# Optimization experiments

Hardware: AMD Instinct MI355X
Metric: run time of the kernel (lower is better)

## Reference

```python
import jax, jax.numpy as jnp
import numpy as np

N_NODES = 50000
N_EDGES = 1600000
D = 128
L = 4
N_GRAPHS = 512


def setup_inputs() -> dict:
    key = jax.random.key(0)
    ks = jax.random.split(key, 8)
    x = jax.random.normal(ks[0], (N_NODES, D), dtype=jnp.float32)
    edge_index = jax.random.randint(ks[1], (2, N_EDGES), 0, N_NODES, dtype=jnp.int64)
    batch = jnp.sort(jax.random.randint(ks[2], (N_NODES,), 0, N_GRAPHS, dtype=jnp.int64))
    # MLP params per GIN layer: Linear(D->D), ReLU, Linear(D->D). Stacked over L layers.
    s = 1.0 / np.sqrt(D)
    Ws1 = jax.random.uniform(ks[3], (L, D, D), jnp.float32, -s, s)
    bs1 = jax.random.uniform(ks[4], (L, D), jnp.float32, -s, s)
    Ws2 = jax.random.uniform(ks[5], (L, D, D), jnp.float32, -s, s)
    bs2 = jax.random.uniform(ks[6], (L, D), jnp.float32, -s, s)
    return {"x": x, "edge_index": edge_index, "batch": batch,
            "Ws1": Ws1, "bs1": bs1, "Ws2": Ws2, "bs2": bs2}


def reference(x, edge_index, batch, Ws1, bs1, Ws2, bs2):
    src, dst = edge_index[0], edge_index[1]
    for l in range(L):
        # GINConv (eps=0): h = MLP(x + sum_{j in N(i)} x_j)
        agg = jax.ops.segment_sum(x[src], dst, num_segments=N_NODES)  # [N, D]
        h = x + agg
        h = jax.nn.relu(h @ Ws1[l] + bs1[l])
        x = h @ Ws2[l] + bs2[l]
    # global_add_pool: segment-sum node features by graph id
    return jax.ops.segment_sum(x, batch, num_segments=N_GRAPHS)  # [G, D]
```

## Files before the change

kernel.cpp:

```cpp
#include <hip/hip_runtime.h>

#define NN 50000
#define NE 1600000
#define DD 128
#define NL 4
#define NG 512
#define BSH 7
#define BMSK 127
#define NBUK 391
#define NBLK 196
#define EPB 8192
#define HN (NBUK * NBLK)
#define HT 150
#define EPT 20
#define CVT_N (NN * DD / 4)
#define PREP_N (NL * DD * DD)

typedef __attribute__((ext_vector_type(8))) short short8;
typedef __attribute__((ext_vector_type(4))) float floatx4;

__device__ __forceinline__ unsigned short f2bf(float f) {
    unsigned int u = __float_as_uint(f);
    u += 0x7fffu + ((u >> 16) & 1u);
    return (unsigned short)(u >> 16);
}
__device__ __forceinline__ float bf2f(unsigned short u) {
    return __uint_as_float(((unsigned int)u) << 16);
}

__global__ __launch_bounds__(512) void prelude_kernel(
    const float* __restrict__ x0, const float* __restrict__ Ws1,
    const float* __restrict__ Ws2, const int* __restrict__ dst,
    unsigned short* __restrict__ xbf, unsigned short* __restrict__ W1T,
    unsigned short* __restrict__ W2T, int* __restrict__ hist) {
    __shared__ int h[NBUK];
    int tid = threadIdx.x, bid = blockIdx.x;
    int gid = bid * 512 + tid;
    for (int idx = gid; idx < CVT_N; idx += NBLK * 512) {
        float4 f = ((const float4*)x0)[idx];
        ushort4 o;
        o.x = f2bf(f.x); o.y = f2bf(f.y); o.z = f2bf(f.z); o.w = f2bf(f.w);
        ((ushort4*)xbf)[idx] = o;
    }
    for (int idx = gid; idx < PREP_N; idx += NBLK * 512) {
        int l = idx >> 14, rem = idx & 16383;
        int k = rem >> 7, n = rem & 127;
        int o = (l << 14) + (n << 7) + k;
        W1T[o] = f2bf(Ws1[idx]);
        W2T[o] = f2bf(Ws2[idx]);
    }
    for (int i = tid; i < NBUK; i += 512) h[i] = 0;
    __syncthreads();
    {
        int base = bid * EPB;
        int end = base + EPB; if (end > NE) end = NE;
        for (int e = base + tid; e < end; e += 512) atomicAdd(&h[dst[e] >> BSH], 1);
    }
    __syncthreads();
    for (int i = tid; i < NBUK; i += 512) hist[i * NBLK + bid] = h[i];
}

__global__ __launch_bounds__(512) void scan_lb_kernel(const int* __restrict__ in,
                                                      int* __restrict__ out,
                                                      unsigned int* __restrict__ tstat,
                                                      int n) {
    __shared__ int s[512];
    int b = blockIdx.x, tid = threadIdx.x;
    int i = b * 512 + tid;
    int v = (i < n) ? in[i] : 0;
    s[tid] = v;
    __syncthreads();
    for (int off = 1; off < 512; off <<= 1) {
        int u = (tid >= off) ? s[tid - off] : 0;
        __syncthreads();
        s[tid] += u;
        __syncthreads();
    }
    int incl = s[tid];
    int agg = s[511];
    if (tid == 0)
        __hip_atomic_store(&tstat[b], 0x80000000u | (unsigned int)agg,
                           __ATOMIC_RELAXED, __HIP_MEMORY_SCOPE_AGENT);
    unsigned int got = 0;
    if (tid < b) {
        unsigned int x = __hip_atomic_load(&tstat[tid], __ATOMIC_RELAXED,
                                           __HIP_MEMORY_SCOPE_AGENT);
        while (!(x & 0x80000000u)) {
            __builtin_amdgcn_s_sleep(1);
            x = __hip_atomic_load(&tstat[tid], __ATOMIC_RELAXED,
                                  __HIP_MEMORY_SCOPE_AGENT);
        }
        got = x & 0x7FFFFFFFu;
    }
    __syncthreads();
    s[tid] = (int)got;
    __syncthreads();
    for (int off = 256; off > 0; off >>= 1) {
        if (tid < off) s[tid] += s[tid + off];
        __syncthreads();
    }
    int carry = s[0];
    if (i < n) out[i] = carry + incl - v;
}

__global__ __launch_bounds__(512) void bscatter_kernel(const int* __restrict__ src,
                                                       const int* __restrict__ dst,
                                                       const int* __restrict__ bkoff,
                                                       int* __restrict__ ebuf) {
    __shared__ int h[NBUK];
    int tid = threadIdx.x;
    for (int i = tid; i < NBUK; i += 512) h[i] = 0;
    __syncthreads();
    int base = blockIdx.x * EPB;
#pragma unroll
    for (int it = 0; it < EPB / 512; it++) {
        int e = base + it * 512 + tid;
        if (e < NE) {
            int d = dst[e];
            int bu = d >> BSH;
            int p = atomicAdd(&h[bu], 1);
            ebuf[bkoff[bu * NBLK + blockIdx.x] + p] = (src[e] << BSH) | (d & BMSK);
        }
    }
}

__global__ __launch_bounds__(256) void bucket_csr_kernel(const int* __restrict__ ebuf,
                                                         const int* __restrict__ bkoff,
                                                         int* __restrict__ rowptr,
                                                         int* __restrict__ rowend,
                                                         int* __restrict__ col) {
    __shared__ int cnt[128], exc[128], ebase[128];
    int b = blockIdx.x, tid = threadIdx.x;
    int segstart = bkoff[b * NBLK];
    int segend = (b < NBUK - 1) ? bkoff[(b + 1) * NBLK] : NE;
    if (tid < 128) cnt[tid] = 0;
    __syncthreads();
    int evr[EPT];
    int rnk[EPT];
#pragma unroll
    for (int j = 0; j < EPT; j++) {
        int i = segstart + tid + j * 256;
        if (i < segend) {
            int ev = ebuf[i];
            evr[j] = ev;
            rnk[j] = atomicAdd(&cnt[ev & BMSK], 1);
        } else {
            evr[j] = -1;
        }
    }
    __syncthreads();
    int v = (tid < 128) ? cnt[tid] : 0;
    if (tid < 128) exc[tid] = v;
    __syncthreads();
    for (int off = 1; off < 128; off <<= 1) {
        int u = (tid < 128 && tid >= off) ? exc[tid - off] : 0;
        __syncthreads();
        if (tid < 128) exc[tid] += u;
        __syncthreads();
    }
    if (tid < 128) {
        int excl = exc[tid] - v;
        ebase[tid] = segstart + excl;
        int node = (b << BSH) + tid;
        if (node < NN) {
            rowptr[node] = segstart + excl;
            rowend[node] = segstart + excl + v;
        }
    }
    __syncthreads();
#pragma unroll
    for (int j = 0; j < EPT; j++) {
        if (evr[j] >= 0) {
            int low = evr[j] & BMSK;
            col[ebase[low] + rnk[j]] = ((unsigned)evr[j]) >> BSH;
        }
    }
}

__global__ __launch_bounds__(256) void agg_kernel(const unsigned short* __restrict__ xbf,
                                                  const int* __restrict__ rowptr,
                                                  const int* __restrict__ rowend,
                                                  const int* __restrict__ col,
                                                  unsigned short* __restrict__ hpre) {
    int g = threadIdx.x >> 4;
    int lane = threadIdx.x & 15;
    int node = blockIdx.x * 16 + g;
    const uint4* base = (const uint4*)xbf;
    float a[8];
    {
        uint4 v = base[node * 16 + lane];
        a[0] = __uint_as_float(v.x << 16); a[1] = __uint_as_float(v.x & 0xFFFF0000u);
        a[2] = __uint_as_float(v.y << 16); a[3] = __uint_as_float(v.y & 0xFFFF0000u);
        a[4] = __uint_as_float(v.z << 16); a[5] = __uint_as_float(v.z & 0xFFFF0000u);
        a[6] = __uint_as_float(v.w << 16); a[7] = __uint_as_float(v.w & 0xFFFF0000u);
    }
    int s = rowptr[node], e = rowend[node];
    int i = s;
    for (; i + 8 <= e; i += 8) {
        uint4 v0 = base[col[i] * 16 + lane];
        uint4 v1 = base[col[i + 1] * 16 + lane];
        uint4 v2 = base[col[i + 2] * 16 + lane];
        uint4 v3 = base[col[i + 3] * 16 + lane];
        uint4 v4 = base[col[i + 4] * 16 + lane];
        uint4 v5 = base[col[i + 5] * 16 + lane];
        uint4 v6 = base[col[i + 6] * 16 + lane];
        uint4 v7 = base[col[i + 7] * 16 + lane];
#define ACC(V)                                                            \
        a[0] += __uint_as_float(V.x << 16); a[1] += __uint_as_float(V.x & 0xFFFF0000u); \
        a[2] += __uint_as_float(V.y << 16); a[3] += __uint_as_float(V.y & 0xFFFF0000u); \
        a[4] += __uint_as_float(V.z << 16); a[5] += __uint_as_float(V.z & 0xFFFF0000u); \
        a[6] += __uint_as_float(V.w << 16); a[7] += __uint_as_float(V.w & 0xFFFF0000u)
        ACC(v0); ACC(v1); ACC(v2); ACC(v3); ACC(v4); ACC(v5); ACC(v6); ACC(v7);
    }
    for (; i < e; i++) {
        uint4 v = base[col[i] * 16 + lane];
        ACC(v);
    }
#undef ACC
    uint4 o;
    o.x = (unsigned int)f2bf(a[0]) | ((unsigned int)f2bf(a[1]) << 16);
    o.y = (unsigned int)f2bf(a[2]) | ((unsigned int)f2bf(a[3]) << 16);
    o.z = (unsigned int)f2bf(a[4]) | ((unsigned int)f2bf(a[5]) << 16);
    o.w = (unsigned int)f2bf(a[6]) | ((unsigned int)f2bf(a[7]) << 16);
    ((uint4*)hpre)[node * 16 + lane] = o;
}

__global__ __launch_bounds__(256) void mlp_kernel(const unsigned short* __restrict__ A,
                                                  const unsigned short* __restrict__ W1,
                                                  const float* __restrict__ b1,
                                                  const unsigned short* __restrict__ W2,
                                                  const float* __restrict__ b2,
                                                  unsigned short* __restrict__ O) {
    __shared__ unsigned short Wl[128 * 128];
    __shared__ unsigned short Hl[128 * 128];
    int tid = threadIdx.x;
    int wg = tid >> 6;
    int lane = tid & 63;
    int quad = lane >> 4;
    int li = lane & 15;
    int mg = wg >> 1, ng = wg & 1;
    int rowb = blockIdx.x * 128;

    short8 xf[4][4];
#pragma unroll
    for (int kk = 0; kk < 4; kk++) {
#pragma unroll
        for (int mi = 0; mi < 4; mi++) {
            int ar = rowb + mg * 64 + mi * 16 + li;
            xf[kk][mi] = (ar < NN)
                ? *(const short8*)(A + (size_t)ar * DD + kk * 32 + quad * 8)
                : (short8){0, 0, 0, 0, 0, 0, 0, 0};
        }
    }

    {
        const uint4* wgl = (const uint4*)W1;
#pragma unroll
        for (int it = 0; it < 8; it++) {
            int idx = it * 256 + tid;
            int n = idx >> 4, kc = idx & 15;
            *(uint4*)&Wl[n * 128 + ((kc * 8) ^ ((n & 7) << 3))] = wgl[idx];
        }
    }
    __syncthreads();

    floatx4 acc[4][4];
#pragma unroll
    for (int tn = 0; tn < 4; tn++)
#pragma unroll
        for (int mi = 0; mi < 4; mi++) acc[tn][mi] = (floatx4){0.f, 0.f, 0.f, 0.f};

#pragma unroll
    for (int kk = 0; kk < 4; kk++) {
        int kc = kk * 32 + quad * 8;
#pragma unroll
        for (int tn = 0; tn < 4; tn++) {
            int wr = ng * 64 + tn * 16 + li;
            short8 wf = *(const short8*)&Wl[wr * 128 + (kc ^ ((wr & 7) << 3))];
#pragma unroll
            for (int mi = 0; mi < 4; mi++)
                acc[tn][mi] = __builtin_amdgcn_mfma_f32_16x16x32_bf16(wf, xf[kk][mi], acc[tn][mi], 0, 0, 0);
        }
    }

#pragma unroll
    for (int tn = 0; tn < 4; tn++) {
        float4 bv = ((const float4*)b1)[ng * 16 + tn * 4 + quad];
#pragma unroll
        for (int mi = 0; mi < 4; mi++) {
            int hr = mg * 64 + mi * 16 + li;
            float v0 = fmaxf(acc[tn][mi][0] + bv.x, 0.f);
            float v1 = fmaxf(acc[tn][mi][1] + bv.y, 0.f);
            float v2 = fmaxf(acc[tn][mi][2] + bv.z, 0.f);
            float v3 = fmaxf(acc[tn][mi][3] + bv.w, 0.f);
            uint2 u;
            u.x = (unsigned int)f2bf(v0) | ((unsigned int)f2bf(v1) << 16);
            u.y = (unsigned int)f2bf(v2) | ((unsigned int)f2bf(v3) << 16);
            int c = (ng * 64 + tn * 16 + quad * 4) ^ ((hr & 7) << 3);
            *(uint2*)&Hl[hr * 128 + c] = u;
        }
    }
    __syncthreads();

    {
        const uint4* wgl = (const uint4*)W2;
#pragma unroll
        for (int it = 0; it < 8; it++) {
            int idx = it * 256 + tid;
            int n = idx >> 4, kc = idx & 15;
            *(uint4*)&Wl[n * 128 + ((kc * 8) ^ ((n & 7) << 3))] = wgl[idx];
        }
    }
    __syncthreads();

#pragma unroll
    for (int tn = 0; tn < 4; tn++)
#pragma unroll
        for (int mi = 0; mi < 4; mi++) acc[tn][mi] = (floatx4){0.f, 0.f, 0.f, 0.f};

#pragma unroll
    for (int kk = 0; kk < 4; kk++) {
        int kc = kk * 32 + quad * 8;
        short8 hf[4];
#pragma unroll
        for (int mi = 0; mi < 4; mi++) {
            int hr = mg * 64 + mi * 16 + li;
            hf[mi] = *(const short8*)&Hl[hr * 128 + (kc ^ ((hr & 7) << 3))];
        }
#pragma unroll
        for (int tn = 0; tn < 4; tn++) {
            int wr = ng * 64 + tn * 16 + li;
            short8 wf = *(const short8*)&Wl[wr * 128 + (kc ^ ((wr & 7) << 3))];
#pragma unroll
            for (int mi = 0; mi < 4; mi++)
                acc[tn][mi] = __builtin_amdgcn_mfma_f32_16x16x32_bf16(wf, hf[mi], acc[tn][mi], 0, 0, 0);
        }
    }

#pragma unroll
    for (int tn = 0; tn < 4; tn++) {
        float4 bv = ((const float4*)b2)[ng * 16 + tn * 4 + quad];
#pragma unroll
        for (int mi = 0; mi < 4; mi++) {
            int m = rowb + mg * 64 + mi * 16 + li;
            if (m < NN) {
                uint2 u;
                u.x = (unsigned int)f2bf(acc[tn][mi][0] + bv.x) |
                      ((unsigned int)f2bf(acc[tn][mi][1] + bv.y) << 16);
                u.y = (unsigned int)f2bf(acc[tn][mi][2] + bv.z) |
                      ((unsigned int)f2bf(acc[tn][mi][3] + bv.w) << 16);
                *(uint2*)&O[(size_t)m * DD + ng * 64 + tn * 16 + quad * 4] = u;
            }
        }
    }
}

__global__ __launch_bounds__(256) void pool_kernel(const unsigned short* __restrict__ x,
                                                   const int* __restrict__ batch,
                                                   float* __restrict__ out) {
    int g = blockIdx.x;
    int lo = 0, hi = NN;
    while (lo < hi) { int mid = (lo + hi) >> 1; if (batch[mid] < g) lo = mid + 1; else hi = mid; }
    int s = lo;
    hi = NN;
    while (lo < hi) { int mid = (lo + hi) >> 1; if (batch[mid] < g + 1) lo = mid + 1; else hi = mid; }
    int e = lo;
    int d = threadIdx.x & 127;
    int half = threadIdx.x >> 7;
    float a0 = 0.f, a1 = 0.f, a2 = 0.f, a3 = 0.f;
    int i = s + half;
    for (; i + 6 < e; i += 8) {
        unsigned short v0 = x[(size_t)i * DD + d];
        unsigned short v1 = x[(size_t)(i + 2) * DD + d];
        unsigned short v2 = x[(size_t)(i + 4) * DD + d];
        unsigned short v3 = x[(size_t)(i + 6) * DD + d];
        a0 += bf2f(v0); a1 += bf2f(v1); a2 += bf2f(v2); a3 += bf2f(v3);
    }
    for (; i < e; i += 2) a0 += bf2f(x[(size_t)i * DD + d]);
    float acc = (a0 + a1) + (a2 + a3);
    __shared__ float red[256];
    red[threadIdx.x] = acc;
    __syncthreads();
    if (threadIdx.x < 128) out[g * DD + d] = red[d] + red[128 + d];
}

extern "C" void kernel_launch(void* const* d_in, const int* in_sizes, int n_in,
                              void* d_out, int out_size, void* d_ws, size_t ws_size,
                              hipStream_t stream) {
    const float* x0 = (const float*)d_in[0];
    const int* edge = (const int*)d_in[1];
    const int* batch = (const int*)d_in[2];
    const float* Ws1 = (const float*)d_in[3];
    const float* bs1 = (const float*)d_in[4];
    const float* Ws2 = (const float*)d_in[5];
    const float* bs2 = (const float*)d_in[6];
    float* out = (float*)d_out;
    const int* src = edge;
    const int* dst = edge + NE;

    char* ws = (char*)d_ws;
    size_t off = 0;
    auto alloc = [&](size_t bytes) {
        void* p = ws + off;
        off += (bytes + 255) & ~(size_t)255;
        return p;
    };
    unsigned short* x0bf = (unsigned short*)alloc((size_t)NN * DD * 2);
    unsigned short* xA = (unsigned short*)alloc((size_t)NN * DD * 2);
    unsigned short* xB = (unsigned short*)alloc((size_t)NN * DD * 2);
    unsigned short* hpre = (unsigned short*)alloc((size_t)NN * DD * 2);
    int* col = (int*)alloc((size_t)NE * 4);
    int* ebuf = (int*)alloc((size_t)NE * 4);
    int* hist = (int*)alloc((size_t)HN * 4);
    int* bkoff = (int*)alloc((size_t)HN * 4);
    int* rowptr = (int*)alloc((size_t)(NN + 1) * 4);
    int* rowend = (int*)alloc((size_t)NN * 4);
    unsigned short* W1T = (unsigned short*)alloc((size_t)NL * DD * DD * 2);
    unsigned short* W2T = (unsigned short*)alloc((size_t)NL * DD * DD * 2);
    unsigned int* tstat = (unsigned int*)alloc(2048);

    (void)hipMemsetAsync(tstat, 0, 2048, stream);
    prelude_kernel<<<NBLK, 512, 0, stream>>>(x0, Ws1, Ws2, dst, x0bf, W1T, W2T, hist);
    scan_lb_kernel<<<HT, 512, 0, stream>>>(hist, bkoff, tstat, HN);
    bscatter_kernel<<<NBLK, 512, 0, stream>>>(src, dst, bkoff, ebuf);
    bucket_csr_kernel<<<NBUK, 256, 0, stream>>>(ebuf, bkoff, rowptr, rowend, col);

    const unsigned short* xin = x0bf;
    unsigned short* bufs[2] = {xA, xB};
    const int mlp_grid = (NN + 127) / 128;
    for (int l = 0; l < NL; l++) {
        agg_kernel<<<NN / 16, 256, 0, stream>>>(xin, rowptr, rowend, col, hpre);
        unsigned short* xout = bufs[l & 1];
        mlp_kernel<<<mlp_grid, 256, 0, stream>>>(hpre, W1T + l * DD * DD, bs1 + l * DD,
                                                 W2T + l * DD * DD, bs2 + l * DD, xout);
        xin = xout;
    }
    pool_kernel<<<NG, 256, 0, stream>>>(xin, batch, out);
}
```

Baseline: 411.0 us.

## Load MLP weights via direct global-to-LDS, batch edge loads, widen prelude grid

Loads each MLP weight tile into LDS with direct global-to-LDS loads (the XOR swizzle moves to the global source address), so the data no longer passes through registers. The prelude and bucket-scatter kernels now read all 16 of their edge indices into registers before doing the shared-memory atomics, giving more loads in flight. The prelude grid grows to 392 blocks for the conversion work, with only the first 196 building the histogram. The direct-to-LDS path depends on the per-wave contiguous destination layout matching the swizzled placement, and the extra register arrays raise register pressure.

```diff
diff --git a/kernel.cpp b/kernel.cpp
--- a/kernel.cpp
+++ b/kernel.cpp
@@ -15,6 +15,7 @@
 #define EPT 20
 #define CVT_N (NN * DD / 4)
 #define PREP_N (NL * DD * DD)
+#define GPRE 392
 
 typedef __attribute__((ext_vector_type(8))) short short8;
 typedef __attribute__((ext_vector_type(4))) float floatx4;
@@ -27,6 +28,11 @@
 __device__ __forceinline__ float bf2f(unsigned short u) {
     return __uint_as_float(((unsigned int)u) << 16);
 }
+
+#define GLOAD_LDS(g, l)                                               \
+    __builtin_amdgcn_global_load_lds(                                 \
+        (const __attribute__((address_space(1))) void*)(g),           \
+        (__attribute__((address_space(3))) void*)(l), 16, 0, 0)
 
 __global__ __launch_bounds__(512) void prelude_kernel(
     const float* __restrict__ x0, const float* __restrict__ Ws1,
@@ -36,28 +42,35 @@
     __shared__ int h[NBUK];
     int tid = threadIdx.x, bid = blockIdx.x;
     int gid = bid * 512 + tid;
-    for (int idx = gid; idx < CVT_N; idx += NBLK * 512) {
+    for (int idx = gid; idx < CVT_N; idx += GPRE * 512) {
         float4 f = ((const float4*)x0)[idx];
         ushort4 o;
         o.x = f2bf(f.x); o.y = f2bf(f.y); o.z = f2bf(f.z); o.w = f2bf(f.w);
         ((ushort4*)xbf)[idx] = o;
     }
-    for (int idx = gid; idx < PREP_N; idx += NBLK * 512) {
+    for (int idx = gid; idx < PREP_N; idx += GPRE * 512) {
         int l = idx >> 14, rem = idx & 16383;
         int k = rem >> 7, n = rem & 127;
         int o = (l << 14) + (n << 7) + k;
         W1T[o] = f2bf(Ws1[idx]);
         W2T[o] = f2bf(Ws2[idx]);
     }
-    for (int i = tid; i < NBUK; i += 512) h[i] = 0;
-    __syncthreads();
-    {
+    if (bid < NBLK) {
+        for (int i = tid; i < NBUK; i += 512) h[i] = 0;
+        __syncthreads();
         int base = bid * EPB;
-        int end = base + EPB; if (end > NE) end = NE;
-        for (int e = base + tid; e < end; e += 512) atomicAdd(&h[dst[e] >> BSH], 1);
-    }
-    __syncthreads();
-    for (int i = tid; i < NBUK; i += 512) hist[i * NBLK + bid] = h[i];
+        int darr[16];
+#pragma unroll
+        for (int it = 0; it < 16; it++) {
+            int e = base + it * 512 + tid;
+            darr[it] = (e < NE) ? dst[e] : -1;
+        }
+#pragma unroll
+        for (int it = 0; it < 16; it++)
+            if (darr[it] >= 0) atomicAdd(&h[darr[it] >> BSH], 1);
+        __syncthreads();
+        for (int i = tid; i < NBUK; i += 512) hist[i * NBLK + bid] = h[i];
+    }
 }
 
 __global__ __launch_bounds__(512) void scan_lb_kernel(const int* __restrict__ in,
@@ -112,14 +125,20 @@
     for (int i = tid; i < NBUK; i += 512) h[i] = 0;
     __syncthreads();
     int base = blockIdx.x * EPB;
-#pragma unroll
-    for (int it = 0; it < EPB / 512; it++) {
+    int sarr[16], darr[16];
+#pragma unroll
+    for (int it = 0; it < 16; it++) {
         int e = base + it * 512 + tid;
-        if (e < NE) {
-            int d = dst[e];
+        if (e < NE) { sarr[it] = src[e]; darr[it] = dst[e]; }
+        else { sarr[it] = 0; darr[it] = -1; }
+    }
+#pragma unroll
+    for (int it = 0; it < 16; it++) {
+        if (darr[it] >= 0) {
+            int d = darr[it];
             int bu = d >> BSH;
             int p = atomicAdd(&h[bu], 1);
-            ebuf[bkoff[bu * NBLK + blockIdx.x] + p] = (src[e] << BSH) | (d & BMSK);
+            ebuf[bkoff[bu * NBLK + blockIdx.x] + p] = (sarr[it] << BSH) | (d & BMSK);
         }
     }
 }
@@ -255,11 +274,13 @@
 
     {
         const uint4* wgl = (const uint4*)W1;
+        int wv = tid >> 6;
+        int l = tid & 63;
 #pragma unroll
         for (int it = 0; it < 8; it++) {
-            int idx = it * 256 + tid;
+            int idx = it * 256 + wv * 64 + l;
             int n = idx >> 4, kc = idx & 15;
-            *(uint4*)&Wl[n * 128 + ((kc * 8) ^ ((n & 7) << 3))] = wgl[idx];
+            GLOAD_LDS(wgl + n * 16 + (kc ^ (n & 7)), &Wl[(it * 256 + wv * 64) * 8]);
         }
     }
     __syncthreads();
@@ -304,11 +325,13 @@
 
     {
         const uint4* wgl = (const uint4*)W2;
+        int wv = tid >> 6;
+        int l = tid & 63;
 #pragma unroll
         for (int it = 0; it < 8; it++) {
-            int idx = it * 256 + tid;
+            int idx = it * 256 + wv * 64 + l;
             int n = idx >> 4, kc = idx & 15;
-            *(uint4*)&Wl[n * 128 + ((kc * 8) ^ ((n & 7) << 3))] = wgl[idx];
+            GLOAD_LDS(wgl + n * 16 + (kc ^ (n & 7)), &Wl[(it * 256 + wv * 64) * 8]);
         }
     }
     __syncthreads();
@@ -420,7 +443,7 @@
     unsigned int* tstat = (unsigned int*)alloc(2048);
 
     (void)hipMemsetAsync(tstat, 0, 2048, stream);
-    prelude_kernel<<<NBLK, 512, 0, stream>>>(x0, Ws1, Ws2, dst, x0bf, W1T, W2T, hist);
+    prelude_kernel<<<GPRE, 512, 0, stream>>>(x0, Ws1, Ws2, dst, x0bf, W1T, W2T, hist);
     scan_lb_kernel<<<HT, 512, 0, stream>>>(hist, bkoff, tstat, HN);
     bscatter_kernel<<<NBLK, 512, 0, stream>>>(src, dst, bkoff, ebuf);
     bucket_csr_kernel<<<NBUK, 256, 0, stream>>>(ebuf, bkoff, rowptr, rowend, col);
```

Measured after the change: 401.8 us. -2.2%, faster.
